# Performance work log

Hardware: AMD Instinct MI355X
Metric: run time of the kernel (lower is better)

Reference implementation:

```python
import math
import jax, jax.numpy as jnp
import numpy as np

D_MODEL = 1024
NUM_SCALES = 4
STATE_SIZE = 16
EXPAND = 2
D_INNER = D_MODEL * EXPAND
D_PER_SCALE = D_INNER // NUM_SCALES
BATCH, SEQ = 4, 4096


def _make_A_log():
    base = np.arange(1, STATE_SIZE + 1, dtype=np.float32)  # (N,)
    parts = [np.broadcast_to(base * (2.0 ** i), (D_PER_SCALE, STATE_SIZE)) for i in range(NUM_SCALES)]
    A = np.concatenate(parts, axis=0)  # (d_inner, N)
    return jnp.asarray(np.log(A))


def setup_inputs() -> dict:
    key = jax.random.key(0)
    ks = jax.random.split(key, 8)
    scale = 0.02
    x = jax.random.normal(ks[0], (BATCH, SEQ, D_MODEL), dtype=jnp.float32)
    W_in = jax.random.normal(ks[1], (2 * D_INNER, D_MODEL), dtype=jnp.float32) * scale
    W_B = jax.random.normal(ks[2], (STATE_SIZE, D_INNER), dtype=jnp.float32) * scale
    W_C = jax.random.normal(ks[3], (STATE_SIZE, D_INNER), dtype=jnp.float32) * scale
    W_dt = jax.random.normal(ks[4], (D_INNER, D_INNER), dtype=jnp.float32) * scale
    # dt bias: log of dt_init ~ Uniform in log-space between 1e-3 and 1e-1
    u = jax.random.uniform(ks[5], (D_INNER,), dtype=jnp.float32)
    b_dt = u * (math.log(0.1) - math.log(0.001)) + math.log(0.001)
    W_out = jax.random.normal(ks[6], (D_MODEL, D_INNER), dtype=jnp.float32) * scale
    A_log = _make_A_log()
    D = jnp.ones((D_INNER,), dtype=jnp.float32)
    output_gate = jnp.zeros((1,), dtype=jnp.float32)
    return {"x": x, "W_in": W_in, "A_log": A_log, "W_B": W_B, "W_C": W_C,
            "W_dt": W_dt, "b_dt": b_dt, "D": D, "output_gate": output_gate, "W_out": W_out}


def _selective_scan(x_ssm, A, B_mat, C_mat, dt):
    # x_ssm: (B,L,d), A: (d,N), B_mat/C_mat: (B,L,N), dt: (B,L,d)
    b, L, d = x_ssm.shape
    N = A.shape[1]
    h0 = jnp.zeros((b, d, N), dtype=jnp.float32)

    def step(h, inp):
        dt_t, B_t, C_t, x_t = inp  # (B,d),(B,N),(B,N),(B,d)
        A_bar = jnp.exp(jnp.minimum(dt_t[..., None] * A, 20.0))       # (B,d,N)
        B_bar = dt_t[..., None] * B_t[:, None, :]                      # (B,d,N)
        h = A_bar * h + B_bar * x_t[..., None]
        y_t = jnp.einsum('bdn,bn->bd', h, C_t)
        return h, y_t

    xs = (jnp.swapaxes(dt, 0, 1), jnp.swapaxes(B_mat, 0, 1),
          jnp.swapaxes(C_mat, 0, 1), jnp.swapaxes(x_ssm, 0, 1))
    _, ys = jax.lax.scan(step, h0, xs)   # ys: (L,B,d)
    return jnp.swapaxes(ys, 0, 1)


def reference(x, W_in, A_log, W_B, W_C, W_dt, b_dt, D, output_gate, W_out):
    xz = jnp.einsum('bld,ed->ble', x, W_in)          # (B,L,2*d_inner)
    x_ssm, z = jnp.split(xz, 2, axis=-1)
    A = -jnp.exp(A_log.astype(jnp.float32))           # (d_inner,N)
    B_mat = jnp.einsum('bld,nd->bln', x_ssm, W_B)
    C_mat = jnp.einsum('bld,nd->bln', x_ssm, W_C)
    dt = jax.nn.softplus(jnp.einsum('bld,ed->ble', x_ssm, W_dt) + b_dt)
    y = _selective_scan(x_ssm.astype(jnp.float32), A,
                        B_mat.astype(jnp.float32), C_mat.astype(jnp.float32),
                        dt.astype(jnp.float32))
    y = y + x_ssm * D[None, None, :]
    y = y * jax.nn.silu(z)
    out = jnp.einsum('ble,de->bld', y, W_out) * jax.nn.sigmoid(output_gate)
    return out
```

## Files before the change

kernel.cpp:

```cpp
#include <hip/hip_runtime.h>
#include <hip/hip_bf16.h>
#include <math.h>

#define D_MODEL 1024
#define D_INNER 2048
#define NSTATE  16
#define BATCH   4
#define SEQ     4096
#define MTOT    (BATCH*SEQ)
#define SDT     2176
#define NCAT    2176
#define NCHUNK  16
#define CLEN    (SEQ/NCHUNK)
#define N1      (2*D_INNER)

typedef __attribute__((ext_vector_type(8))) __bf16 bf16x8;
typedef __attribute__((ext_vector_type(4))) float f32x4;

__device__ __forceinline__ float b2f(unsigned short u){
  return __uint_as_float(((unsigned int)u) << 16);
}
__device__ __forceinline__ unsigned short f2b(float f){
  unsigned int u = __float_as_uint(f);
  u = (u + 0x7FFFu + ((u >> 16) & 1u)) >> 16;
  return (unsigned short)u;
}
__device__ __forceinline__ float softplus_f(float x){
  float r = log1pf(__expf(-fabsf(x)));
  return x > 0.f ? x + r : r;
}

__device__ __forceinline__ void async16(unsigned short* lds, const unsigned short* g){
  __builtin_amdgcn_global_load_lds(
      (const __attribute__((address_space(1))) unsigned int*)g,
      (__attribute__((address_space(3))) unsigned int*)lds, 16, 0, 0);
}

__global__ void cvt_f2b_kernel(const float* __restrict__ src,
                               unsigned short* __restrict__ dst){
  int i = (blockIdx.x * 256 + threadIdx.x) * 4;
  float4 v = *(const float4*)(src + i);
  *(ushort2*)(dst + i)     = (ushort2){f2b(v.x), f2b(v.y)};
  *(ushort2*)(dst + i + 2) = (ushort2){f2b(v.z), f2b(v.w)};
}

__global__ void concat_w_kernel(const float* __restrict__ Wdt,
                                const float* __restrict__ WB,
                                const float* __restrict__ WC,
                                unsigned short* __restrict__ Wcat){
  int idx = blockIdx.x * 256 + threadIdx.x;
  int row = idx >> 9;
  int q   = idx & 511;
  float4 v;
  if      (row < 2048) v = *(const float4*)(Wdt + ((size_t)row * 2048 + q * 4));
  else if (row < 2064) v = *(const float4*)(WB  + ((size_t)(row - 2048) * 2048 + q * 4));
  else if (row < 2080) v = *(const float4*)(WC  + ((size_t)(row - 2064) * 2048 + q * 4));
  else                 v = make_float4(0.f, 0.f, 0.f, 0.f);
  unsigned short* p = Wcat + (size_t)idx * 4;
  *(ushort2*)(p)     = (ushort2){f2b(v.x), f2b(v.y)};
  *(ushort2*)(p + 2) = (ushort2){f2b(v.z), f2b(v.w)};
}

template<int MODE, int K, int GX>
__global__ __launch_bounds__(512, 1) void gemm_bt(
    const unsigned short* __restrict__ A,
    const unsigned short* __restrict__ W,
    unsigned short* __restrict__ o0,
    unsigned short* __restrict__ o1,
    float* __restrict__ of,
    const float* __restrict__ bias)
{
  const int tid  = threadIdx.x;
  const int lane = tid & 63;
  const int w    = tid >> 6;
  const int wm   = w >> 1;
  const int wn   = w & 1;
  const int m16  = lane & 15, q = lane >> 4;

  constexpr int NWG = GX * (MTOT / 256);
  int flat = blockIdx.y * GX + blockIdx.x;
  flat = (flat & 7) * (NWG >> 3) + (flat >> 3);
  const int bm = flat / GX;
  const int bn = flat - bm * GX;

  __shared__ unsigned short sA[2][16384];
  __shared__ unsigned short sB[2][8192];

  f32x4 acc[4][4];
  #pragma unroll
  for (int i = 0; i < 4; i++)
    #pragma unroll
    for (int j = 0; j < 4; j++) acc[i][j] = (f32x4){0.f, 0.f, 0.f, 0.f};

  const int ch = (tid & 7) ^ ((tid >> 3) & 7);
  const unsigned short* Ag = A + (size_t)(bm * 256 + (tid >> 3)) * K + ch * 8;
  const unsigned short* Wg = W + (size_t)(bn * 128 + (tid >> 3)) * K + ch * 8;

#define STAGE_A(buf, h, t) do { \
    async16(&sA[buf][(h)*8192 + w*512],        Ag + (size_t)((h)*128    )*K + (t)*64); \
    async16(&sA[buf][(h)*8192 + 4096 + w*512], Ag + (size_t)((h)*128 + 64)*K + (t)*64); \
  } while(0)
#define STAGE_B(buf, t) do { \
    async16(&sB[buf][w*512],        Wg + (size_t)(t)*64); \
    async16(&sB[buf][4096 + w*512], Wg + (size_t)64*K + (t)*64); \
  } while(0)

#define LDA(dst, buf) do { \
    _Pragma("unroll") for (int mt = 0; mt < 4; mt++) \
    _Pragma("unroll") for (int kk = 0; kk < 2; kk++) { \
      const int row_ = wm*64 + mt*16 + m16; \
      dst[mt][kk] = *(const bf16x8*)&sA[buf][row_*64 + (((kk*4 + q) ^ (m16 & 7)) << 3)]; \
    } } while(0)
#define LDB(dst, buf, nh) do { \
    _Pragma("unroll") for (int nt = 0; nt < 2; nt++) \
    _Pragma("unroll") for (int kk = 0; kk < 2; kk++) { \
      const int row_ = wn*64 + (nh)*32 + nt*16 + m16; \
      dst[nt][kk] = *(const bf16x8*)&sB[buf][row_*64 + (((kk*4 + q) ^ (m16 & 7)) << 3)]; \
    } } while(0)

#define MMAQ(Aa, Bb, NH) do { \
    __builtin_amdgcn_s_setprio(1); \
    _Pragma("unroll") for (int kk = 0; kk < 2; kk++) \
    _Pragma("unroll") for (int mt = 0; mt < 4; mt++) \
    _Pragma("unroll") for (int nt = 0; nt < 2; nt++) \
      acc[mt][(NH)*2 + nt] = __builtin_amdgcn_mfma_f32_16x16x32_bf16( \
          Aa[mt][kk], Bb[nt][kk], acc[mt][(NH)*2 + nt], 0, 0, 0); \
    __builtin_amdgcn_s_setprio(0); \
  } while(0)

#define BAR()  asm volatile("s_barrier" ::: "memory")
#define LGK0() asm volatile("s_waitcnt lgkmcnt(0)" ::: "memory")

  STAGE_A(0, 0, 0); STAGE_A(0, 1, 0); STAGE_B(0, 0);
  STAGE_A(1, 0, 1); STAGE_A(1, 1, 1);
  asm volatile("s_waitcnt vmcnt(4)" ::: "memory");
  BAR();

  auto run_iter = [&](int t0, bool last) {
    bf16x8 a[4][2], b[2][2];
    LDA(a, 0); LDB(b, 0, 0);
    STAGE_B(1, t0 + 1);
    BAR(); LGK0();
    MMAQ(a, b, 0);
    BAR();
    LDB(b, 0, 1);
    if (!last) { STAGE_A(0, 0, t0 + 2); STAGE_A(0, 1, t0 + 2); }
    BAR(); LGK0();
    MMAQ(a, b, 1);
    if (last) asm volatile("s_waitcnt vmcnt(0)" ::: "memory");
    else      asm volatile("s_waitcnt vmcnt(4)" ::: "memory");
    BAR();
    LDA(a, 1); LDB(b, 1, 0);
    if (!last) STAGE_B(0, t0 + 2);
    BAR(); LGK0();
    MMAQ(a, b, 0);
    BAR();
    LDB(b, 1, 1);
    if (!last) { STAGE_A(1, 0, t0 + 3); STAGE_A(1, 1, t0 + 3); }
    BAR(); LGK0();
    MMAQ(a, b, 1);
    if (!last) asm volatile("s_waitcnt vmcnt(4)" ::: "memory");
    BAR();
  };

  constexpr int NIT = K >> 7;
  #pragma unroll 1
  for (int j = 0; j < NIT - 1; j++) run_iter(2 * j, false);
  run_iter(2 * (NIT - 1), true);

  float gscale = 1.f;
  if (MODE == 2) gscale = 1.f / (1.f + __expf(-bias[0]));

  const int r0 = bm * 256 + wm * 64 + (q << 2);
  const int c0 = bn * 128 + wn * 64 + m16;
  #pragma unroll
  for (int mt = 0; mt < 4; mt++) {
    #pragma unroll
    for (int nt = 0; nt < 4; nt++) {
      const int col = c0 + nt * 16;
      #pragma unroll
      for (int i = 0; i < 4; i++) {
        const int row = r0 + mt * 16 + i;
        float v = acc[mt][nt][i];
        if (MODE == 0) {
          if (col < D_INNER) o0[(size_t)row * D_INNER + col] = f2b(v);
          else               o1[(size_t)row * D_INNER + (col - D_INNER)] = f2b(v);
        } else if (MODE == 1) {
          if (col < D_INNER) v = softplus_f(v + bias[col]);
          o0[(size_t)row * SDT + col] = f2b(v);
        } else {
          of[(size_t)row * D_MODEL + col] = v * gscale;
        }
      }
    }
  }
#undef STAGE_A
#undef STAGE_B
#undef LDA
#undef LDB
#undef MMAQ
#undef BAR
#undef LGK0
}

__global__ __launch_bounds__(256) void scan_passA(
    const unsigned short* __restrict__ dtBC,
    const unsigned short* __restrict__ xs,
    const float* __restrict__ Alog,
    float* __restrict__ Pb, float* __restrict__ Sb)
{
  const int d = blockIdx.x * 256 + threadIdx.x;
  const int b = blockIdx.y;
  const int c = blockIdx.z;

  float a[NSTATE];
  #pragma unroll
  for (int n = 0; n < NSTATE; n++) a[n] = -__expf(Alog[d * NSTATE + n]);

  float P[NSTATE], S[NSTATE];
  #pragma unroll
  for (int n = 0; n < NSTATE; n++) { P[n] = 1.f; S[n] = 0.f; }

  __shared__ float sB[16][16];
  const size_t bL = (size_t)b * SEQ;
  const int t0c = c * CLEN;
  const int lt = threadIdx.x >> 4, ln = threadIdx.x & 15;

  for (int t0 = t0c; t0 < t0c + CLEN; t0 += 16) {
    __syncthreads();
    sB[lt][ln] = b2f(dtBC[(bL + t0 + lt) * SDT + 2048 + ln]);
    __syncthreads();
    for (int tt = 0; tt < 16; tt++) {
      const size_t rw = bL + t0 + tt;
      const float dt = b2f(dtBC[rw * SDT + d]);
      const float x  = b2f(xs[rw * D_INNER + d]);
      const float dtx = dt * x;
      #pragma unroll
      for (int n = 0; n < NSTATE; n++) {
        const float ab = __expf(dt * a[n]);
        P[n] *= ab;
        S[n] = ab * S[n] + dtx * sB[tt][n];
      }
    }
  }
  const size_t base = (((size_t)c * BATCH + b) * D_INNER + d) * NSTATE;
  #pragma unroll
  for (int n = 0; n < NSTATE; n += 4) {
    *(f32x4*)&Pb[base + n] = (f32x4){P[n], P[n+1], P[n+2], P[n+3]};
    *(f32x4*)&Sb[base + n] = (f32x4){S[n], S[n+1], S[n+2], S[n+3]};
  }
}

__global__ __launch_bounds__(256) void scan_passB(float* __restrict__ Pb,
                                                  const float* __restrict__ Sb)
{
  const size_t j = (size_t)blockIdx.x * 256 + threadIdx.x;
  const size_t stride = (size_t)BATCH * D_INNER * NSTATE;
  float h = 0.f;
  for (int c = 0; c < NCHUNK; c++) {
    const size_t idx = (size_t)c * stride + j;
    const float p = Pb[idx];
    const float s = Sb[idx];
    Pb[idx] = h;
    h = p * h + s;
  }
}

__global__ __launch_bounds__(256) void scan_passC(
    const unsigned short* __restrict__ dtBC,
    const unsigned short* __restrict__ xs,
    const unsigned short* __restrict__ zb,
    const float* __restrict__ Alog,
    const float* __restrict__ Dv,
    const float* __restrict__ Hb,
    unsigned short* __restrict__ yb)
{
  const int d = blockIdx.x * 256 + threadIdx.x;
  const int b = blockIdx.y;
  const int c = blockIdx.z;

  float a[NSTATE];
  #pragma unroll
  for (int n = 0; n < NSTATE; n++) a[n] = -__expf(Alog[d * NSTATE + n]);

  float h[NSTATE];
  const size_t base = (((size_t)c * BATCH + b) * D_INNER + d) * NSTATE;
  #pragma unroll
  for (int n = 0; n < NSTATE; n += 4) {
    f32x4 v = *(const f32x4*)&Hb[base + n];
    h[n] = v.x; h[n+1] = v.y; h[n+2] = v.z; h[n+3] = v.w;
  }
  const float Dd = Dv[d];

  __shared__ float sB[16][16];
  __shared__ float sC[16][16];
  const size_t bL = (size_t)b * SEQ;
  const int t0c = c * CLEN;
  const int lt = threadIdx.x >> 4, ln = threadIdx.x & 15;

  for (int t0 = t0c; t0 < t0c + CLEN; t0 += 16) {
    __syncthreads();
    {
      const size_t rwb = (bL + t0 + lt) * SDT + 2048;
      sB[lt][ln] = b2f(dtBC[rwb + ln]);
      sC[lt][ln] = b2f(dtBC[rwb + 16 + ln]);
    }
    __syncthreads();
    for (int tt = 0; tt < 16; tt++) {
      const size_t rw = bL + t0 + tt;
      const float dt = b2f(dtBC[rw * SDT + d]);
      const float x  = b2f(xs[rw * D_INNER + d]);
      const float z  = b2f(zb[rw * D_INNER + d]);
      const float dtx = dt * x;
      float y = 0.f;
      #pragma unroll
      for (int n = 0; n < NSTATE; n++) {
        const float ab = __expf(dt * a[n]);
        h[n] = ab * h[n] + dtx * sB[tt][n];
        y += h[n] * sC[tt][n];
      }
      y = (y + x * Dd) * (z / (1.f + __expf(-z)));
      yb[rw * D_INNER + d] = f2b(y);
    }
  }
}

extern "C" void kernel_launch(void* const* d_in, const int* in_sizes, int n_in,
                              void* d_out, int out_size, void* d_ws, size_t ws_size,
                              hipStream_t stream)
{
  const float* x    = (const float*)d_in[0];
  const float* Win  = (const float*)d_in[1];
  const float* Alog = (const float*)d_in[2];
  const float* WB   = (const float*)d_in[3];
  const float* WC   = (const float*)d_in[4];
  const float* Wdt  = (const float*)d_in[5];
  const float* bdt  = (const float*)d_in[6];
  const float* Dv   = (const float*)d_in[7];
  const float* gate = (const float*)d_in[8];
  const float* Wout = (const float*)d_in[9];
  float* outp = (float*)d_out;

  char* ws = (char*)d_ws;
  unsigned short* xs    = (unsigned short*)(ws + 0);
  unsigned short* zy    = (unsigned short*)(ws + 67108864);
  unsigned short* dtBC  = (unsigned short*)(ws + 134217728);
  unsigned short* Winb  = (unsigned short*)(ws + 205520896);
  unsigned short* Woutb = (unsigned short*)(ws + 213909504);

  char* ob = (char*)d_out;
  float* Pb = (float*)(ob + 0);
  float* Sb = (float*)(ob + 8388608);
  unsigned short* Wcatb = (unsigned short*)(ob + 16777216);
  unsigned short* xb    = (unsigned short*)(ob + 33554432);

  cvt_f2b_kernel<<<16384, 256, 0, stream>>>(x, xb);
  cvt_f2b_kernel<<<4096, 256, 0, stream>>>(Win, Winb);
  cvt_f2b_kernel<<<2048, 256, 0, stream>>>(Wout, Woutb);
  concat_w_kernel<<<(NCAT * D_INNER / 4) / 256, 256, 0, stream>>>(Wdt, WB, WC, Wcatb);

  gemm_bt<0, D_MODEL, N1 / 128><<<dim3(N1 / 128, MTOT / 256), 512, 0, stream>>>(
      xb, Winb, xs, zy, nullptr, nullptr);
  gemm_bt<1, D_INNER, NCAT / 128><<<dim3(NCAT / 128, MTOT / 256), 512, 0, stream>>>(
      xs, Wcatb, dtBC, nullptr, nullptr, bdt);
  scan_passA<<<dim3(D_INNER / 256, BATCH, NCHUNK), 256, 0, stream>>>(
      dtBC, xs, Alog, Pb, Sb);
  scan_passB<<<(BATCH * D_INNER * NSTATE) / 256, 256, 0, stream>>>(Pb, Sb);
  scan_passC<<<dim3(D_INNER / 256, BATCH, NCHUNK), 256, 0, stream>>>(
      dtBC, xs, zy, Alog, Dv, Pb, zy);
  gemm_bt<2, D_INNER, D_MODEL / 128><<<dim3(D_MODEL / 128, MTOT / 256), 512, 0, stream>>>(
      zy, Woutb, nullptr, nullptr, outp, gate);
}
```

Measured before the change: 1.101 ms.

## Fold dt/B/C projection weights into input projection via precomputed weight product

Precomputes the product of the concatenated dt/B/C weights with the x-half of W_in, so dt, B and C are produced directly from x in one widened input-projection GEMM. This removes the separate K=2048 GEMM over x_ssm and its reread of the intermediate activations. It adds a small weight-product GEMM, a transpose kernel and a zero fill. The extra bf16 rounding of the combined weights changes numerics slightly.

```diff
diff --git a/kernel.cpp b/kernel.cpp
--- a/kernel.cpp
+++ b/kernel.cpp
@@ -9,7 +9,8 @@
 #define SEQ     4096
 #define MTOT    (BATCH*SEQ)
 #define SDT     2176
-#define NCAT    2176
+#define NCATP   2304
+#define NBIG    6272
 #define NCHUNK  16
 #define CLEN    (SEQ/NCHUNK)
 #define N1      (2*D_INNER)
@@ -61,12 +62,43 @@
   *(ushort2*)(p + 2) = (ushort2){f2b(v.z), f2b(v.w)};
 }
 
-template<int MODE, int K, int GX>
+__global__ __launch_bounds__(256) void transpose_cvt_kernel(
+    const float* __restrict__ Win, unsigned short* __restrict__ WxT){
+  __shared__ float t[64][65];
+  const int e0 = blockIdx.x * 64;
+  const int k0 = blockIdx.y * 64;
+  const int r  = threadIdx.x >> 2;
+  const int q  = threadIdx.x & 3;
+  #pragma unroll
+  for (int jj = 0; jj < 4; jj++){
+    float4 v = *(const float4*)&Win[(size_t)(e0 + r) * 1024 + k0 + q*16 + jj*4];
+    t[r][q*16 + jj*4 + 0] = v.x; t[r][q*16 + jj*4 + 1] = v.y;
+    t[r][q*16 + jj*4 + 2] = v.z; t[r][q*16 + jj*4 + 3] = v.w;
+  }
+  __syncthreads();
+  #pragma unroll
+  for (int jj = 0; jj < 2; jj++){
+    ushort4 o;
+    o.x = f2b(t[q*16 + jj*8 + 0][r]); o.y = f2b(t[q*16 + jj*8 + 1][r]);
+    o.z = f2b(t[q*16 + jj*8 + 2][r]); o.w = f2b(t[q*16 + jj*8 + 3][r]);
+    *(ushort4*)&WxT[(size_t)(k0 + r) * 2048 + e0 + q*16 + jj*8] = o;
+    o.x = f2b(t[q*16 + jj*8 + 4][r]); o.y = f2b(t[q*16 + jj*8 + 5][r]);
+    o.z = f2b(t[q*16 + jj*8 + 6][r]); o.w = f2b(t[q*16 + jj*8 + 7][r]);
+    *(ushort4*)&WxT[(size_t)(k0 + r) * 2048 + e0 + q*16 + jj*8 + 4] = o;
+  }
+}
+
+__global__ void zfill_kernel(unsigned short* __restrict__ p){
+  p[blockIdx.x * 256 + threadIdx.x] = 0;
+}
+
+template<int MODE, int K, int GX, int GY>
 __global__ __launch_bounds__(512, 1) void gemm_bt(
     const unsigned short* __restrict__ A,
     const unsigned short* __restrict__ W,
     unsigned short* __restrict__ o0,
     unsigned short* __restrict__ o1,
+    unsigned short* __restrict__ o2,
     float* __restrict__ of,
     const float* __restrict__ bias)
 {
@@ -77,7 +109,7 @@
   const int wn   = w & 1;
   const int m16  = lane & 15, q = lane >> 4;
 
-  constexpr int NWG = GX * (MTOT / 256);
+  constexpr int NWG = GX * GY;
   int flat = blockIdx.y * GX + blockIdx.x;
   flat = (flat & 7) * (NWG >> 3) + (flat >> 3);
   const int bm = flat / GX;
@@ -183,13 +215,15 @@
         const int row = r0 + mt * 16 + i;
         float v = acc[mt][nt][i];
         if (MODE == 0) {
-          if (col < D_INNER) o0[(size_t)row * D_INNER + col] = f2b(v);
-          else               o1[(size_t)row * D_INNER + (col - D_INNER)] = f2b(v);
-        } else if (MODE == 1) {
-          if (col < D_INNER) v = softplus_f(v + bias[col]);
-          o0[(size_t)row * SDT + col] = f2b(v);
+          if      (col < 2048) o0[(size_t)row * D_INNER + col] = f2b(v);
+          else if (col < 4096) o1[(size_t)row * D_INNER + (col - 2048)] = f2b(v);
+          else if (col < 6144) o2[(size_t)row * SDT + (col - 4096)] =
+                                   f2b(softplus_f(v + bias[col - 4096]));
+          else if (col < 6176) o2[(size_t)row * SDT + 2048 + (col - 6144)] = f2b(v);
+        } else if (MODE == 2) {
+          of[(size_t)row * D_MODEL + col] = v * gscale;
         } else {
-          of[(size_t)row * D_MODEL + col] = v * gscale;
+          if (row < 2080) o0[(size_t)row * D_MODEL + col] = f2b(v);
         }
       }
     }
@@ -345,29 +379,34 @@
   unsigned short* xs    = (unsigned short*)(ws + 0);
   unsigned short* zy    = (unsigned short*)(ws + 67108864);
   unsigned short* dtBC  = (unsigned short*)(ws + 134217728);
-  unsigned short* Winb  = (unsigned short*)(ws + 205520896);
+  unsigned short* WxT   = (unsigned short*)(ws + 205520896);
   unsigned short* Woutb = (unsigned short*)(ws + 213909504);
 
   char* ob = (char*)d_out;
   float* Pb = (float*)(ob + 0);
   float* Sb = (float*)(ob + 8388608);
-  unsigned short* Wcatb = (unsigned short*)(ob + 16777216);
+  unsigned short* Acomp = (unsigned short*)(ob + 0);
+  unsigned short* Wcomb = (unsigned short*)(ob + 16777216);
   unsigned short* xb    = (unsigned short*)(ob + 33554432);
 
   cvt_f2b_kernel<<<16384, 256, 0, stream>>>(x, xb);
-  cvt_f2b_kernel<<<4096, 256, 0, stream>>>(Win, Winb);
+  cvt_f2b_kernel<<<4096, 256, 0, stream>>>(Win, Wcomb);
   cvt_f2b_kernel<<<2048, 256, 0, stream>>>(Wout, Woutb);
-  concat_w_kernel<<<(NCAT * D_INNER / 4) / 256, 256, 0, stream>>>(Wdt, WB, WC, Wcatb);
-
-  gemm_bt<0, D_MODEL, N1 / 128><<<dim3(N1 / 128, MTOT / 256), 512, 0, stream>>>(
-      xb, Winb, xs, zy, nullptr, nullptr);
-  gemm_bt<1, D_INNER, NCAT / 128><<<dim3(NCAT / 128, MTOT / 256), 512, 0, stream>>>(
-      xs, Wcatb, dtBC, nullptr, nullptr, bdt);
+  concat_w_kernel<<<(NCATP * D_INNER / 4) / 256, 256, 0, stream>>>(Wdt, WB, WC, Acomp);
+  transpose_cvt_kernel<<<dim3(32, 16), 256, 0, stream>>>(Win, WxT);
+  zfill_kernel<<<384, 256, 0, stream>>>(Wcomb + (size_t)6176 * 1024);
+
+  gemm_bt<3, 2048, 8, 9><<<dim3(8, 9), 512, 0, stream>>>(
+      Acomp, WxT, Wcomb + (size_t)4096 * 1024, nullptr, nullptr, nullptr, nullptr);
+
+  gemm_bt<0, D_MODEL, NBIG / 128, MTOT / 256><<<dim3(NBIG / 128, MTOT / 256), 512, 0, stream>>>(
+      xb, Wcomb, xs, zy, dtBC, nullptr, bdt);
+
   scan_passA<<<dim3(D_INNER / 256, BATCH, NCHUNK), 256, 0, stream>>>(
       dtBC, xs, Alog, Pb, Sb);
   scan_passB<<<(BATCH * D_INNER * NSTATE) / 256, 256, 0, stream>>>(Pb, Sb);
   scan_passC<<<dim3(D_INNER / 256, BATCH, NCHUNK), 256, 0, stream>>>(
       dtBC, xs, zy, Alog, Dv, Pb, zy);
-  gemm_bt<2, D_INNER, D_MODEL / 128><<<dim3(D_MODEL / 128, MTOT / 256), 512, 0, stream>>>(
-      zy, Woutb, nullptr, nullptr, outp, gate);
-}
+  gemm_bt<2, D_INNER, D_MODEL / 128, MTOT / 256><<<dim3(D_MODEL / 128, MTOT / 256), 512, 0, stream>>>(
+      zy, Woutb, nullptr, nullptr, nullptr, outp, gate);
+}
```

New measurement: 1.177 ms. +6.8%, slower.
